# Performance work log

Hardware: AMD Instinct MI355X
Metric: run time of the kernel (lower is better)

## Reference

```python
import jax, jax.numpy as jnp
import numpy as np

V, E, H = 32000, 1024, 1024  # vocab, wemb, enc
T1, B = 129, 64


def setup_inputs() -> dict:
    key = jax.random.key(0)
    ks = jax.random.split(key, 6)
    sH = 1.0 / np.sqrt(H)
    data = jax.random.randint(ks[0], (T1, B), 0, V)
    mask = jnp.ones((T1, B), jnp.float32)
    emb = jax.random.normal(ks[1], (V, E), jnp.float32) * 0.02
    W_ih = jax.random.normal(ks[2], (E, 4 * H), jnp.float32) * sH
    W_hh = jax.random.normal(ks[3], (H, 4 * H), jnp.float32) * sH
    b = jnp.zeros((4 * H,), jnp.float32)
    Wr = jax.random.normal(ks[4], (E, H), jnp.float32) * sH  # readout: Linear(H -> E), torch weight (out,in)
    br = jnp.zeros((E,), jnp.float32)
    bd = jnp.zeros((V,), jnp.float32)  # decoder bias (weight tied to emb)
    return {"data": data, "mask": mask, "emb": emb, "W_ih": W_ih, "W_hh": W_hh,
            "b": b, "Wr": Wr, "br": br, "bd": bd}


def reference(data, mask, emb, W_ih, W_hh, b, Wr, br, bd):
    x_data = data[:-1]          # [Tx, B]
    y_data = data[1:]           # [Tx, B]
    m_all = mask[1:]            # note: source uses mask[1:] for BOTH x_mask and y_mask
    Tx, Bn = x_data.shape

    def step(carry, xs):
        ht, ct, loss = carry
        tx, ty, mt = xs                      # [B], [B], [B]
        x = emb[tx]                          # [B, E] embedding lookup
        g = x @ W_ih + ht @ W_hh + b         # [B, 4H]
        i, f, gg, o = jnp.split(g, 4, axis=1)
        i = jax.nn.sigmoid(i); f = jax.nn.sigmoid(f); o = jax.nn.sigmoid(o)
        gg = jnp.tanh(gg)
        cn = f * ct + i * gg
        hn = o * jnp.tanh(cn)
        mm = mt[:, None]
        ht2 = mm * hn + (1.0 - mm) * ht      # masked state update
        ct2 = mm * cn + (1.0 - mm) * ct
        out = ht2 @ Wr.T + br                # readout [B, E]
        logit = out @ emb.T + bd             # tied decoder [B, V]
        logp = jax.nn.log_softmax(logit, axis=1)
        nll = -jnp.take_along_axis(logp, ty[:, None], axis=1)[:, 0]
        loss = loss + jnp.mean(nll * mt)     # loss_reduction == 'org'
        return (ht2, ct2, loss), None

    init = (jnp.zeros((Bn, H), jnp.float32), jnp.zeros((Bn, H), jnp.float32),
            jnp.zeros((), jnp.float32))
    (_, _, loss), _ = jax.lax.scan(step, init, (x_data, y_data, m_all))
    return loss / Bn
```

## Files before the change

kernel.cpp:

```cpp
#include <hip/hip_runtime.h>
#include <stdint.h>

#define V_  32000
#define E_  1024
#define H_  1024
#define B_  64
#define T_  128
#define MROWS (T_ * B_)
#define NCB_ 250
#define NTG  32
#define ITEMS_PER_TG 258
#define TOTAL_ITEMS (NTG * ITEMS_PER_TG)

typedef __bf16 bf16x8 __attribute__((ext_vector_type(8)));
typedef float  f32x4  __attribute__((ext_vector_type(4)));

__device__ __forceinline__ uint16_t f2b(float f) {
  uint32_t u = __builtin_bit_cast(uint32_t, f);
  return (uint16_t)((u + 0x7fffu + ((u >> 16) & 1u)) >> 16);
}
__device__ __forceinline__ float b2f(uint16_t h) {
  uint32_t u = ((uint32_t)h) << 16;
  return __builtin_bit_cast(float, u);
}
__device__ __forceinline__ float fsig_(float x) {
  return __builtin_amdgcn_rcpf(1.0f + __expf(-x));
}
__device__ __forceinline__ float ftanh_(float x) {
  return 2.0f * __builtin_amdgcn_rcpf(1.0f + __expf(-2.0f * x)) - 1.0f;
}

__device__ __forceinline__ void gload16(const uint16_t* g, uint16_t* l) {
  __builtin_amdgcn_global_load_lds(
      (const __attribute__((address_space(1))) uint32_t*)g,
      (__attribute__((address_space(3))) uint32_t*)l,
      16, 0, 0);
}


__global__ void k_cvt(const float* __restrict__ src, uint16_t* __restrict__ dst, int n4) {
  int i = blockIdx.x * blockDim.x + threadIdx.x;
  int st = gridDim.x * blockDim.x;
  for (; i < n4; i += st) {
    float4 v = ((const float4*)src)[i];
    ushort4 o;
    o.x = f2b(v.x); o.y = f2b(v.y); o.z = f2b(v.z); o.w = f2b(v.w);
    ((ushort4*)dst)[i] = o;
  }
}

__global__ void k_tcvt(const float* __restrict__ src, uint16_t* __restrict__ dst,
                       int R, int C, int dstStride, int dstOff) {
  __shared__ float tile[32][33];
  int c0 = blockIdx.x * 32, r0 = blockIdx.y * 32;
  int tx = threadIdx.x, ty = threadIdx.y;
  for (int j = 0; j < 32; j += 8)
    tile[ty + j][tx] = src[(size_t)(r0 + ty + j) * C + c0 + tx];
  __syncthreads();
  for (int j = 0; j < 32; j += 8)
    dst[(size_t)(c0 + ty + j) * dstStride + dstOff + r0 + tx] = f2b(tile[tx][ty + j]);
}

__global__ void k_zero(uint4* p, int n) {
  int i = blockIdx.x * blockDim.x + threadIdx.x;
  int st = gridDim.x * blockDim.x;
  uint4 z = {0, 0, 0, 0};
  for (; i < n; i += st) p[i] = z;
}

__global__ __launch_bounds__(256) void k_xw(
    const int* __restrict__ data, const uint16_t* __restrict__ embB,
    const uint16_t* __restrict__ Wcat,
    const float* __restrict__ bias, uint16_t* __restrict__ xAll)
{
  __shared__ uint16_t lA[128 * 64];
  __shared__ uint16_t lB[128 * 64];

  int tid = threadIdx.x;
  int w = tid >> 6, l = tid & 63, lr = l & 15, lg = l >> 4;
  int wr = w >> 1, wc = w & 1;
  int m0 = blockIdx.x * 128;
  int n0 = blockIdx.y * 128;

  int stRow = l >> 3;
  int kswz  = ((l & 7) * 8) ^ ((stRow & 7) << 3);
  const uint16_t* aSrc[4];
  const uint16_t* bSrc[4];
#pragma unroll
  for (int cc = 0; cc < 4; ++cc) {
    int tok = data[m0 + w * 32 + cc * 8 + stRow];
    aSrc[cc] = embB + (size_t)tok * 1024 + kswz;
    bSrc[cc] = Wcat + (size_t)(n0 + w * 32 + cc * 8 + stRow) * 2048 + kswz;
  }

  f32x4 acc[4][4] = {};

  for (int kt = 0; kt < 1024; kt += 64) {
#pragma unroll
    for (int cc = 0; cc < 4; ++cc) {
      gload16(aSrc[cc] + kt, &lA[(w * 4 + cc) * 512]);
      gload16(bSrc[cc] + kt, &lB[(w * 4 + cc) * 512]);
    }
    __syncthreads();
#pragma unroll
    for (int ksub = 0; ksub < 2; ++ksub) {
      bf16x8 af[4], bfr[4];
      int ke = ksub * 32 + lg * 8;
#pragma unroll
      for (int mi = 0; mi < 4; ++mi) {
        int row = wr * 64 + mi * 16 + lr;
        af[mi] = *(const bf16x8*)&lA[row * 64 + (ke ^ ((row & 7) << 3))];
      }
#pragma unroll
      for (int ni = 0; ni < 4; ++ni) {
        int row = wc * 64 + ni * 16 + lr;
        bfr[ni] = *(const bf16x8*)&lB[row * 64 + (ke ^ ((row & 7) << 3))];
      }
#pragma unroll
      for (int mi = 0; mi < 4; ++mi)
#pragma unroll
        for (int ni = 0; ni < 4; ++ni)
          acc[mi][ni] = __builtin_amdgcn_mfma_f32_16x16x32_bf16(af[mi], bfr[ni], acc[mi][ni], 0, 0, 0);
    }
    __syncthreads();
  }

  float bv[4];
#pragma unroll
  for (int ni = 0; ni < 4; ++ni) bv[ni] = bias[n0 + wc * 64 + ni * 16 + lr];
#pragma unroll
  for (int mi = 0; mi < 4; ++mi)
#pragma unroll
    for (int ni = 0; ni < 4; ++ni) {
      int row = wr * 64 + mi * 16 + lg * 4;
      int col = n0 + wc * 64 + ni * 16 + lr;
#pragma unroll
      for (int r = 0; r < 4; ++r)
        xAll[(size_t)(m0 + row + r) * 4096 + col] = f2b(acc[mi][ni][r] + bv[ni]);
    }
}

__global__ __launch_bounds__(512) void k_mega(
    const uint16_t* __restrict__ xAll, const uint16_t* __restrict__ Wcat,
    const float* __restrict__ mask, uint16_t* __restrict__ hAll,
    uint32_t* __restrict__ flags,
    const uint16_t* __restrict__ embB, const uint16_t* __restrict__ WrB,
    const float* __restrict__ br, const float* __restrict__ bd,
    uint16_t* __restrict__ outAll, float2* __restrict__ part,
    uint32_t* __restrict__ projDone, uint32_t* __restrict__ workCtr)
{
  __shared__ alignas(16) char smem[151552];

  int tid = threadIdx.x;
  int blk = blockIdx.x;
  int w = tid >> 6, l = tid & 63, lr = l & 15, lg = l >> 4;

  if (blk < 64) {
    uint16_t* wh    = (uint16_t*)smem;
    uint16_t* xs0   = (uint16_t*)(smem + 131072);
    uint16_t* xs1   = (uint16_t*)(smem + 139264);
    uint16_t* hp0   = (uint16_t*)(smem + 147456);
    uint16_t* hp1   = (uint16_t*)(smem + 149504);
    uint16_t* xsb[2] = {xs0, xs1};
    uint16_t* hpb[2] = {hp0, hp1};

    int u0 = blk * 16;

    for (int it = 0; it < 16; ++it) {
      int ch = it * 512 + tid;
      int c  = ch >> 7;
      int kb = (ch & 127) * 16;
      int gRow = (c & 3) * 1024 + u0 + (c >> 2);
      uint4 v = *(const uint4*)((const char*)Wcat + (size_t)gRow * 4096 + 2048 + kb);
      *(uint4*)((char*)wh + c * 2048 + (kb ^ ((c & 7) << 4))) = v;
    }

    int wm = w >> 1, wn = w & 1;
    int q = lr & 3;

    const char* wb0 = (const char*)wh + (size_t)(wn * 32 + lr) * 2048;
    const char* wb1 = (const char*)wh + (size_t)(wn * 32 + 16 + lr) * 2048;
    int xr = (lr & 7) << 4;

    int sRow = tid >> 3, sQ = (tid >> 1) & 3, sHalf = tid & 1;
    const uint16_t* xSrc = xAll + (size_t)sRow * 4096 + sQ * 1024 + u0 + sHalf * 8;
    int xDstOff = sRow * 64 + sQ * 16 + sHalf * 8;
    int xoBase = (wm * 16 + lg * 4) * 64 + q * 16 + wn * 8 + (lr >> 2);
    int rot = (blk >> 4) & 3;

    float cR[2][4] = {}, hR[2][4] = {};

    uint4 xwReg = *(const uint4*)xSrc;
    *(uint4*)&xsb[0][xDstOff] = xwReg;
    xwReg = *(const uint4*)(xSrc + (size_t)1 * B_ * 4096);
    __syncthreads();

    int cur = 0;
    for (int t = 0; t < T_; ++t) {
      if (t + 1 < T_) *(uint4*)&xsb[cur ^ 1][xDstOff] = xwReg;
      if (t + 2 < T_) xwReg = *(const uint4*)(xSrc + (size_t)(t + 2) * B_ * 4096);

      float xwv[2][4], mm_[4];
#pragma unroll
      for (int ni = 0; ni < 2; ++ni)
#pragma unroll
        for (int r = 0; r < 4; ++r)
          xwv[ni][r] = b2f(xsb[cur][xoBase + r * 64 + ni * 4]);
#pragma unroll
      for (int r = 0; r < 4; ++r)
        mm_[r] = mask[(t + 1) * B_ + wm * 16 + lg * 4 + r];

      const uint16_t* aH = hAll + (size_t)t * (B_ * H_) + (size_t)(wm * 16 + lr) * H_ + lg * 8;

      f32x4 acc0 = {0.f, 0.f, 0.f, 0.f}, acc1 = {0.f, 0.f, 0.f, 0.f};
      unsigned long long bal = 0;
      if (t > 0) {
        uint32_t f = __hip_atomic_load(&flags[l], __ATOMIC_RELAXED, __HIP_MEMORY_SCOPE_AGENT);
        bal = __ballot((int)(f >= (uint32_t)t));
      }
      for (int cc = 0; cc < 4; ++cc) {
        int ch = (cc + rot) & 3;
        if (t > 0) {
          unsigned long long need = 0xFFFFull << (ch * 16);
          while ((bal & need) != need) {
            __builtin_amdgcn_s_sleep(1);
            uint32_t f = __hip_atomic_load(&flags[l], __ATOMIC_RELAXED, __HIP_MEMORY_SCOPE_AGENT);
            bal = __ballot((int)(f >= (uint32_t)t));
          }
          asm volatile("" ::: "memory");
        }
#pragma unroll
        for (int k2 = 0; k2 < 8; ++k2) {
          int ks = ch * 8 + k2;
          bf16x8 a = *(const bf16x8*)(aH + ks * 32);
          int ko = (ks * 64 + lg * 16) ^ xr;
          bf16x8 b0 = *(const bf16x8*)(wb0 + ko);
          bf16x8 b1 = *(const bf16x8*)(wb1 + ko);
          acc0 = __builtin_amdgcn_mfma_f32_16x16x32_bf16(a, b0, acc0, 0, 0, 0);
          acc1 = __builtin_amdgcn_mfma_f32_16x16x32_bf16(a, b1, acc1, 0, 0, 0);
        }
      }

#pragma unroll
      for (int ni = 0; ni < 2; ++ni) {
        f32x4 accv = ni ? acc1 : acc0;
#pragma unroll
        for (int r = 0; r < 4; ++r) {
          float v0 = accv[r] + xwv[ni][r];
          float v1 = __shfl_xor(v0, 1, 64);
          float v2 = __shfl_xor(v0, 2, 64);
          float v3 = __shfl_xor(v0, 3, 64);
          float gi = (q == 0) ? v0 : (q == 1) ? v1 : (q == 2) ? v2 : v3;
          float gf = (q == 1) ? v0 : (q == 0) ? v1 : (q == 3) ? v2 : v3;
          float gg = (q == 2) ? v0 : (q == 3) ? v1 : (q == 0) ? v2 : v3;
          float go = (q == 3) ? v0 : (q == 2) ? v1 : (q == 1) ? v2 : v3;
          gi = fsig_(gi); gf = fsig_(gf); gg = ftanh_(gg); go = fsig_(go);
          float cn = gf * cR[ni][r] + gi * gg;
          float hn = go * ftanh_(cn);
          float mm = mm_[r];
          cR[ni][r] = mm * cn + (1.f - mm) * cR[ni][r];
          hR[ni][r] = mm * hn + (1.f - mm) * hR[ni][r];
          if (q == 0)
            hpb[cur][(wm * 16 + lg * 4 + r) * 16 + wn * 8 + ni * 4 + (lr >> 2)] = f2b(hR[ni][r]);
        }
      }

      __syncthreads();

      if (w == 0) {
        const unsigned long long* hp = (const unsigned long long*)hpb[cur];
        unsigned long long* hd =
            (unsigned long long*)(hAll + (size_t)(t + 1) * (B_ * H_) + (size_t)l * H_ + u0);
#pragma unroll
        for (int j = 0; j < 4; ++j)
          __hip_atomic_store(hd + j, hp[l * 4 + j],
                             __ATOMIC_RELAXED, __HIP_MEMORY_SCOPE_AGENT);
        asm volatile("s_waitcnt vmcnt(0)" ::: "memory");
        if (l == 0)
          __hip_atomic_store(&flags[blk], (uint32_t)(t + 1),
                             __ATOMIC_RELAXED, __HIP_MEMORY_SCOPE_AGENT);
      }
      cur ^= 1;
    }
  } else {
    uint16_t* lA  = (uint16_t*)smem;
    uint16_t* lB  = (uint16_t*)(smem + 32768);
    float2*   cm  = (float2*)(smem + 49152);
    uint32_t* sId = (uint32_t*)(smem + 53248);

    int stRow = l >> 3;
    int kswz  = ((l & 7) * 8) ^ ((stRow & 7) << 3);
    int wr = w >> 1;
    int wc = w & 1;

    for (;;) {
      __syncthreads();
      if (tid == 0)
        *sId = __hip_atomic_fetch_add(workCtr, 1u, __ATOMIC_RELAXED, __HIP_MEMORY_SCOPE_AGENT);
      __syncthreads();
      uint32_t id = *sId;
      if (id >= TOTAL_ITEMS) break;
      int tg = (int)(id / ITEMS_PER_TG), sub = (int)(id % ITEMS_PER_TG);
      int t0 = tg * 4;
      bool isProj = (sub < 8);

      const uint16_t* Abase;
      const uint16_t* Bbase;
      const float* biasp;
      if (isProj) {
        uint32_t tv = (uint32_t)(t0 + 4);
        while (!__all((int)(__hip_atomic_load(&flags[l], __ATOMIC_RELAXED,
                                              __HIP_MEMORY_SCOPE_AGENT) >= tv)))
          __builtin_amdgcn_s_sleep(8);
        asm volatile("" ::: "memory");
        Abase = hAll + (size_t)(t0 + 1) * (B_ * H_);
        Bbase = WrB + (size_t)(sub * 128) * 1024;
        biasp = br + sub * 128;
      } else {
        while (__hip_atomic_load(&projDone[tg], __ATOMIC_RELAXED,
                                 __HIP_MEMORY_SCOPE_AGENT) < 8u)
          __builtin_amdgcn_s_sleep(8);
        asm volatile("" ::: "memory");
        Abase = outAll + (size_t)t0 * B_ * 1024;
        Bbase = embB + (size_t)(sub - 8) * 128 * 1024;
        biasp = bd + (sub - 8) * 128;
      }

      const uint16_t* aS = Abase + (size_t)(w * 32 + stRow) * 1024 + kswz;
      const uint16_t* bS = Bbase + (size_t)(w * 16 + stRow) * 1024 + kswz;

      f32x4 acc[4][4] = {};
      for (int kt = 0; kt < 1024; kt += 64) {
#pragma unroll
        for (int cc = 0; cc < 4; ++cc)
          gload16(aS + (size_t)cc * 8 * 1024 + kt, &lA[(w * 4 + cc) * 512]);
#pragma unroll
        for (int cc = 0; cc < 2; ++cc)
          gload16(bS + (size_t)cc * 8 * 1024 + kt, &lB[(w * 2 + cc) * 512]);
        __syncthreads();
#pragma unroll
        for (int ksub = 0; ksub < 2; ++ksub) {
          int ke = ksub * 32 + lg * 8;
          bf16x8 af[4], bfr[4];
#pragma unroll
          for (int mi = 0; mi < 4; ++mi) {
            int row = wr * 64 + mi * 16 + lr;
            af[mi] = *(const bf16x8*)&lA[row * 64 + (ke ^ ((row & 7) << 3))];
          }
#pragma unroll
          for (int ni = 0; ni < 4; ++ni) {
            int row = wc * 64 + ni * 16 + lr;
            bfr[ni] = *(const bf16x8*)&lB[row * 64 + (ke ^ ((row & 7) << 3))];
          }
#pragma unroll
          for (int mi = 0; mi < 4; ++mi)
#pragma unroll
            for (int ni = 0; ni < 4; ++ni)
              acc[mi][ni] = __builtin_amdgcn_mfma_f32_16x16x32_bf16(af[mi], bfr[ni], acc[mi][ni], 0, 0, 0);
        }
        __syncthreads();
      }

      float bv[4];
#pragma unroll
      for (int ni = 0; ni < 4; ++ni) bv[ni] = biasp[wc * 64 + ni * 16 + lr];

      if (isProj) {
        int e0 = sub * 128;
        uint16_t* opack = lA;
#pragma unroll
        for (int chunk = 0; chunk < 4; ++chunk) {
          if (wr == chunk) {
#pragma unroll
            for (int mi = 0; mi < 4; ++mi)
#pragma unroll
              for (int ni = 0; ni < 4; ++ni)
#pragma unroll
                for (int r = 0; r < 4; ++r)
                  opack[(mi * 16 + lg * 4 + r) * 128 + wc * 64 + ni * 16 + lr]
                    = f2b(acc[mi][ni][r] + bv[ni]);
          }
          __syncthreads();
          const unsigned long long* op = (const unsigned long long*)opack;
#pragma unroll
          for (int j = 0; j < 4; ++j) {
            int g = j * 512 + tid;
            int row = g >> 5, seg = g & 31;
            unsigned long long* od =
                (unsigned long long*)(outAll + ((size_t)(t0 + chunk) * B_ + row) * 1024 + e0) + seg;
            __hip_atomic_store(od, op[g], __ATOMIC_RELAXED, __HIP_MEMORY_SCOPE_AGENT);
          }
          __syncthreads();
        }
        asm volatile("s_waitcnt vmcnt(0)" ::: "memory");
        __syncthreads();
        if (tid == 0)
          __hip_atomic_fetch_add(&projDone[tg], 1u, __ATOMIC_RELAXED, __HIP_MEMORY_SCOPE_AGENT);
      } else {
        int nc = sub - 8;
#pragma unroll
        for (int mi = 0; mi < 4; ++mi) {
#pragma unroll
          for (int r = 0; r < 4; ++r) {
            float mx = -1e30f;
#pragma unroll
            for (int ni = 0; ni < 4; ++ni) { acc[mi][ni][r] += bv[ni]; mx = fmaxf(mx, acc[mi][ni][r]); }
#pragma unroll
            for (int d = 1; d < 16; d <<= 1) mx = fmaxf(mx, __shfl_xor(mx, d, 64));
            float s = 0.f;
#pragma unroll
            for (int ni = 0; ni < 4; ++ni) s += expf(acc[mi][ni][r] - mx);
#pragma unroll
            for (int d = 1; d < 16; d <<= 1) s += __shfl_xor(s, d, 64);
            if (lr == 0) cm[wc * 256 + wr * 64 + mi * 16 + lg * 4 + r] = make_float2(mx, s);
          }
        }
        __syncthreads();
        if (tid < 256) {
          float2 p0 = cm[tid], p1 = cm[256 + tid];
          float M = fmaxf(p0.x, p1.x);
          float S = p0.y * expf(p0.x - M) + p1.y * expf(p1.x - M);
          part[(size_t)nc * MROWS + (size_t)t0 * B_ + tid] = make_float2(M, S);
        }
      }
    }
  }
}

__global__ __launch_bounds__(256) void k_tgt(
    const uint16_t* __restrict__ outAll, const uint16_t* __restrict__ embB,
    const float* __restrict__ bd, const int* __restrict__ data, float* __restrict__ tgt)
{
  int w = threadIdx.x >> 6, l = threadIdx.x & 63;
  int row = blockIdx.x * 4 + w;
  int t = row >> 6, b = row & 63;
  int ty = data[(t + 1) * B_ + b];
  const uint16_t* a = outAll + (size_t)row * E_;
  const uint16_t* e = embB + (size_t)ty * E_;
  float s = 0.f;
#pragma unroll
  for (int i0 = 0; i0 < 2; ++i0) {
    int i = (l + i0 * 64) * 8;
    bf16x8 av = *(const bf16x8*)(a + i);
    bf16x8 ev = *(const bf16x8*)(e + i);
#pragma unroll
    for (int j = 0; j < 8; ++j) s += (float)av[j] * (float)ev[j];
  }
#pragma unroll
  for (int d = 1; d < 64; d <<= 1) s += __shfl_xor(s, d, 64);
  if (l == 0) tgt[row] = s + bd[ty];
}

__global__ __launch_bounds__(256) void k_lse(
    const float2* __restrict__ part, const float* __restrict__ tgt,
    const float* __restrict__ mask, float* __restrict__ rowNll)
{
  int w = threadIdx.x >> 6, l = threadIdx.x & 63;
  int row = blockIdx.x * 4 + w;
  float m = -1e30f, s = 0.f;
  for (int cc = l; cc < NCB_; cc += 64) {
    float2 v = part[(size_t)cc * MROWS + row];
    float M = fmaxf(m, v.x);
    s = s * expf(m - M) + v.y * expf(v.x - M);
    m = M;
  }
#pragma unroll
  for (int d = 1; d < 64; d <<= 1) {
    float om = __shfl_xor(m, d, 64);
    float os = __shfl_xor(s, d, 64);
    float M = fmaxf(m, om);
    s = s * expf(m - M) + os * expf(om - M);
    m = M;
  }
  if (l == 0) {
    int t = row >> 6, b = row & 63;
    float nll = (m + logf(s)) - tgt[row];
    rowNll[row] = nll * mask[(t + 1) * B_ + b];
  }
}

__global__ void k_final2(const float* __restrict__ rowNll, float* __restrict__ out) {
  __shared__ float red[256];
  float s = 0.f;
  for (int i = threadIdx.x; i < MROWS; i += 256) s += rowNll[i];
  red[threadIdx.x] = s;
  __syncthreads();
  for (int st = 128; st > 0; st >>= 1) {
    if ((int)threadIdx.x < st) red[threadIdx.x] += red[threadIdx.x + st];
    __syncthreads();
  }
  if (threadIdx.x == 0) out[0] = red[0] / (float)(B_ * B_);
}

extern "C" void kernel_launch(void* const* d_in, const int* in_sizes, int n_in,
                              void* d_out, int out_size, void* d_ws, size_t ws_size,
                              hipStream_t stream)
{
  const int*   data = (const int*)  d_in[0];
  const float* mask = (const float*)d_in[1];
  const float* emb  = (const float*)d_in[2];
  const float* W_ih = (const float*)d_in[3];
  const float* W_hh = (const float*)d_in[4];
  const float* bias = (const float*)d_in[5];
  const float* Wr   = (const float*)d_in[6];
  const float* br   = (const float*)d_in[7];
  const float* bd   = (const float*)d_in[8];
  (void)in_sizes; (void)n_in; (void)out_size; (void)ws_size;

  char* ws = (char*)d_ws;
  size_t off = 0;
  auto alloc = [&](size_t bytes) -> char* {
    char* p = ws + off;
    off += (bytes + 255) & ~(size_t)255;
    return p;
  };
  uint16_t* embB   = (uint16_t*)alloc((size_t)V_ * E_ * 2);
  uint16_t* Wcat   = (uint16_t*)alloc((size_t)4 * H_ * 2048 * 2);
  uint16_t* WrB    = (uint16_t*)alloc((size_t)E_ * H_ * 2);
  uint16_t* hAll   = (uint16_t*)alloc((size_t)(T_ + 1) * B_ * H_ * 2);
  uint16_t* xAll   = (uint16_t*)alloc((size_t)MROWS * 4096 * 2);
  uint16_t* outAll = (uint16_t*)alloc((size_t)MROWS * E_ * 2);
  float2*   part   = (float2*)  alloc((size_t)NCB_ * MROWS * 8);
  float*    tgt    = (float*)   alloc((size_t)MROWS * 4);
  float*    rowNll = (float*)   alloc((size_t)MROWS * 4);
  uint32_t* syncb  = (uint32_t*)alloc(4096);
  uint32_t* flags    = syncb;
  uint32_t* projDone = syncb + 128;
  uint32_t* workCtr  = syncb + 512;

  k_cvt <<<2048, 256, 0, stream>>>(emb, embB, V_ * E_ / 4);
  k_cvt <<<256,  256, 0, stream>>>(Wr, WrB, E_ * H_ / 4);
  k_tcvt<<<dim3(4 * H_ / 32, E_ / 32), dim3(32, 8), 0, stream>>>(W_ih, Wcat, E_, 4 * H_, 2048, 0);
  k_tcvt<<<dim3(4 * H_ / 32, H_ / 32), dim3(32, 8), 0, stream>>>(W_hh, Wcat, H_, 4 * H_, 2048, 1024);
  k_zero<<<32, 256, 0, stream>>>((uint4*)hAll, B_ * H_ * 2 / 16);
  k_zero<<<1, 256, 0, stream>>>((uint4*)syncb, 4096 / 16);

  k_xw<<<dim3(MROWS / 128, 4096 / 128), 256, 0, stream>>>(data, embB, Wcat, bias, xAll);

  k_mega<<<256, 512, 0, stream>>>(xAll, Wcat, mask, hAll, flags,
                                  embB, WrB, br, bd, outAll, part,
                                  projDone, workCtr);

  k_tgt   <<<MROWS / 4, 256, 0, stream>>>(outAll, embB, bd, data, tgt);
  k_lse   <<<MROWS / 4, 256, 0, stream>>>(part, tgt, mask, rowNll);
  k_final2<<<1, 256, 0, stream>>>(rowNll, (float*)d_out);
}
```

Baseline: 2.187 ms.

## Replace flag polling with sentinel-validated hidden-state loads in recurrent step

Per-chunk polling of producer flags before reading h is removed. h buffers for steps 1..T are pre-filled with a -inf bf16 sentinel, and consumers load chunks with relaxed atomic 64-bit loads, re-polling only while any sentinel is present. Loads for the next chunk are issued before the current chunk's MFMAs to overlap latency, and the chunk rotation now uses blk&3. This drops a flag round-trip and fence per step but adds a large sentinel fill of the h buffer. Correctness depends on 64-bit stores being seen atomically and on no real h value equalling the sentinel pattern.

```diff
diff --git a/kernel.cpp b/kernel.cpp
--- a/kernel.cpp
+++ b/kernel.cpp
@@ -11,6 +11,7 @@
 #define NTG  32
 #define ITEMS_PER_TG 258
 #define TOTAL_ITEMS (NTG * ITEMS_PER_TG)
+#define SENT64 0xFF80FF80FF80FF80ull
 
 typedef __bf16 bf16x8 __attribute__((ext_vector_type(8)));
 typedef float  f32x4  __attribute__((ext_vector_type(4)));
@@ -35,6 +36,42 @@
       (const __attribute__((address_space(1))) uint32_t*)g,
       (__attribute__((address_space(3))) uint32_t*)l,
       16, 0, 0);
+}
+
+__device__ __forceinline__ void ld_chunk(const unsigned long long* aH8, int ch,
+                                         unsigned long long (&dst)[16]) {
+#pragma unroll
+  for (int k2 = 0; k2 < 8; ++k2) {
+    size_t o = (size_t)(ch * 8 + k2) * 8;
+    dst[k2 * 2]     = __hip_atomic_load(aH8 + o,     __ATOMIC_RELAXED, __HIP_MEMORY_SCOPE_AGENT);
+    dst[k2 * 2 + 1] = __hip_atomic_load(aH8 + o + 1, __ATOMIC_RELAXED, __HIP_MEMORY_SCOPE_AGENT);
+  }
+}
+__device__ __forceinline__ void val_chunk(const unsigned long long* aH8, int ch,
+                                          unsigned long long (&dst)[16]) {
+  for (;;) {
+    bool bad = false;
+#pragma unroll
+    for (int j = 0; j < 16; ++j) bad |= (dst[j] == SENT64);
+    if (!__any((int)bad)) break;
+    __builtin_amdgcn_s_sleep(1);
+    ld_chunk(aH8, ch, dst);
+  }
+}
+__device__ __forceinline__ void mfma_chunk(const unsigned long long (&src)[16], int ch,
+                                           const char* wb0, const char* wb1, int lg, int xr,
+                                           f32x4& acc0, f32x4& acc1) {
+#pragma unroll
+  for (int k2 = 0; k2 < 8; ++k2) {
+    int ks = ch * 8 + k2;
+    union { unsigned long long u[2]; bf16x8 v; } cv;
+    cv.u[0] = src[k2 * 2]; cv.u[1] = src[k2 * 2 + 1];
+    int ko = (ks * 64 + lg * 16) ^ xr;
+    bf16x8 b0 = *(const bf16x8*)(wb0 + ko);
+    bf16x8 b1 = *(const bf16x8*)(wb1 + ko);
+    acc0 = __builtin_amdgcn_mfma_f32_16x16x32_bf16(cv.v, b0, acc0, 0, 0, 0);
+    acc1 = __builtin_amdgcn_mfma_f32_16x16x32_bf16(cv.v, b1, acc1, 0, 0, 0);
+  }
 }
 
 
@@ -61,10 +98,10 @@
     dst[(size_t)(c0 + ty + j) * dstStride + dstOff + r0 + tx] = f2b(tile[tx][ty + j]);
 }
 
-__global__ void k_zero(uint4* p, int n) {
+__global__ void k_fill(uint4* p, int n, uint32_t val) {
   int i = blockIdx.x * blockDim.x + threadIdx.x;
   int st = gridDim.x * blockDim.x;
-  uint4 z = {0, 0, 0, 0};
+  uint4 z = {val, val, val, val};
   for (; i < n; i += st) p[i] = z;
 }
 
@@ -186,7 +223,8 @@
     const uint16_t* xSrc = xAll + (size_t)sRow * 4096 + sQ * 1024 + u0 + sHalf * 8;
     int xDstOff = sRow * 64 + sQ * 16 + sHalf * 8;
     int xoBase = (wm * 16 + lg * 4) * 64 + q * 16 + wn * 8 + (lr >> 2);
-    int rot = (blk >> 4) & 3;
+    int rot = blk & 3;
+    int c0 = rot, c1 = (rot + 1) & 3, c2 = (rot + 2) & 3, c3 = (rot + 3) & 3;
 
     float cR[2][4] = {}, hR[2][4] = {};
 
@@ -210,36 +248,25 @@
       for (int r = 0; r < 4; ++r)
         mm_[r] = mask[(t + 1) * B_ + wm * 16 + lg * 4 + r];
 
-      const uint16_t* aH = hAll + (size_t)t * (B_ * H_) + (size_t)(wm * 16 + lr) * H_ + lg * 8;
+      const unsigned long long* aH8 =
+          (const unsigned long long*)(hAll + (size_t)t * (B_ * H_)) +
+          (size_t)(wm * 16 + lr) * 256 + lg * 2;
 
       f32x4 acc0 = {0.f, 0.f, 0.f, 0.f}, acc1 = {0.f, 0.f, 0.f, 0.f};
-      unsigned long long bal = 0;
-      if (t > 0) {
-        uint32_t f = __hip_atomic_load(&flags[l], __ATOMIC_RELAXED, __HIP_MEMORY_SCOPE_AGENT);
-        bal = __ballot((int)(f >= (uint32_t)t));
-      }
-      for (int cc = 0; cc < 4; ++cc) {
-        int ch = (cc + rot) & 3;
-        if (t > 0) {
-          unsigned long long need = 0xFFFFull << (ch * 16);
-          while ((bal & need) != need) {
-            __builtin_amdgcn_s_sleep(1);
-            uint32_t f = __hip_atomic_load(&flags[l], __ATOMIC_RELAXED, __HIP_MEMORY_SCOPE_AGENT);
-            bal = __ballot((int)(f >= (uint32_t)t));
-          }
-          asm volatile("" ::: "memory");
-        }
-#pragma unroll
-        for (int k2 = 0; k2 < 8; ++k2) {
-          int ks = ch * 8 + k2;
-          bf16x8 a = *(const bf16x8*)(aH + ks * 32);
-          int ko = (ks * 64 + lg * 16) ^ xr;
-          bf16x8 b0 = *(const bf16x8*)(wb0 + ko);
-          bf16x8 b1 = *(const bf16x8*)(wb1 + ko);
-          acc0 = __builtin_amdgcn_mfma_f32_16x16x32_bf16(a, b0, acc0, 0, 0, 0);
-          acc1 = __builtin_amdgcn_mfma_f32_16x16x32_bf16(a, b1, acc1, 0, 0, 0);
-        }
-      }
+      unsigned long long hv0[16], hv1[16];
+
+      ld_chunk(aH8, c0, hv0);
+      ld_chunk(aH8, c1, hv1);
+      val_chunk(aH8, c0, hv0);
+      mfma_chunk(hv0, c0, wb0, wb1, lg, xr, acc0, acc1);
+      ld_chunk(aH8, c2, hv0);
+      val_chunk(aH8, c1, hv1);
+      mfma_chunk(hv1, c1, wb0, wb1, lg, xr, acc0, acc1);
+      ld_chunk(aH8, c3, hv1);
+      val_chunk(aH8, c2, hv0);
+      mfma_chunk(hv0, c2, wb0, wb1, lg, xr, acc0, acc1);
+      val_chunk(aH8, c3, hv1);
+      mfma_chunk(hv1, c3, wb0, wb1, lg, xr, acc0, acc1);
 
 #pragma unroll
       for (int ni = 0; ni < 2; ++ni) {
@@ -532,8 +559,10 @@
   k_cvt <<<256,  256, 0, stream>>>(Wr, WrB, E_ * H_ / 4);
   k_tcvt<<<dim3(4 * H_ / 32, E_ / 32), dim3(32, 8), 0, stream>>>(W_ih, Wcat, E_, 4 * H_, 2048, 0);
   k_tcvt<<<dim3(4 * H_ / 32, H_ / 32), dim3(32, 8), 0, stream>>>(W_hh, Wcat, H_, 4 * H_, 2048, 1024);
-  k_zero<<<32, 256, 0, stream>>>((uint4*)hAll, B_ * H_ * 2 / 16);
-  k_zero<<<1, 256, 0, stream>>>((uint4*)syncb, 4096 / 16);
+  k_fill<<<32,   256, 0, stream>>>((uint4*)hAll, B_ * H_ * 2 / 16, 0u);
+  k_fill<<<2048, 256, 0, stream>>>((uint4*)(hAll + (size_t)B_ * H_),
+                                   T_ * B_ * H_ * 2 / 16, 0xFF80FF80u);
+  k_fill<<<1,    256, 0, stream>>>((uint4*)syncb, 4096 / 16, 0u);
 
   k_xw<<<dim3(MROWS / 128, 4096 / 128), 256, 0, stream>>>(data, embB, Wcat, bias, xAll);
 
```

New measurement: 2.777 ms. +27.0%, slower.
